# Performance work log

Hardware: AMD Instinct MI355X
Metric: run time of the kernel (lower is better)

Reference implementation:

```python
import jax, jax.numpy as jnp
import numpy as np

T, B, S, D = 128, 32, 100, 256  # targetL, batch, sourceL, output_size
EPS = 1e-6

def setup_inputs() -> dict:
    key = jax.random.key(0)
    ks = jax.random.split(key, 9)
    sc = 0.05  # weight init scale
    inp = {
        'prev_layer': jax.random.normal(ks[0], (T, B, D), dtype=jnp.float32),
        'hidden': jax.random.normal(ks[1], (B, D), dtype=jnp.float32),
        'enc_output': jax.random.normal(ks[2], (T * B, S, D), dtype=jnp.float32),
        # linear weights (layer_norm=True -> no biases on linears)
        'W_in': jax.random.normal(ks[3], (D, 3 * D), dtype=jnp.float32) * sc,
        'W_hid': jax.random.normal(ks[4], (D, D), dtype=jnp.float32) * sc,
        'W_ctx': jax.random.normal(ks[5], (D, D), dtype=jnp.float32) * sc,
        'W_enc': jax.random.normal(ks[6], (D, D), dtype=jnp.float32) * sc,
        'W_q': jax.random.normal(ks[7], (D, D), dtype=jnp.float32) * sc,   # MLPAttention query proj
        'v_att': jax.random.normal(ks[8], (D,), dtype=jnp.float32) * sc,  # MLPAttention score vector
        # layernorm affine params
        'g_pre': jnp.ones(3 * D, jnp.float32), 'b_pre': jnp.zeros(3 * D, jnp.float32),
        'g_enc': jnp.ones(D, jnp.float32), 'b_enc': jnp.zeros(D, jnp.float32),
        'g_h': jnp.ones(D, jnp.float32), 'b_h': jnp.zeros(D, jnp.float32),
        'g_c': jnp.ones(D, jnp.float32), 'b_c': jnp.zeros(D, jnp.float32),
        'g_q': jnp.ones(D, jnp.float32), 'b_q': jnp.zeros(D, jnp.float32),
    }
    return inp

def _ln(x, g, b):
    m = jnp.mean(x, axis=-1, keepdims=True)
    v = jnp.mean((x - m) ** 2, axis=-1, keepdims=True)
    return g * (x - m) / jnp.sqrt(v + EPS) + b

def reference(prev_layer, hidden, enc_output, W_in, W_hid, W_ctx, W_enc, W_q, v_att,
              g_pre, b_pre, g_enc, b_enc, g_h, b_h, g_c, b_c, g_q, b_q):
    Tl, Bb, Dd = prev_layer.shape
    # input / encoder projections (dropout=0 -> identity)
    preact = _ln(prev_layer @ W_in, g_pre, b_pre)        # [T,B,3D]
    pctx = _ln(enc_output @ W_enc, g_enc, b_enc)         # [T*B,S,D]
    z, h_gate, x_t = jnp.split(preact, 3, axis=-1)
    z = jax.nn.sigmoid(z)
    h_gate = jax.nn.sigmoid(h_gate)
    # SRU-style elementwise linear recurrence over time
    def step(h, zx):
        zt, xt = zx
        s = (1.0 - zt) * h + zt * xt
        return s, s
    final_h, ss = jax.lax.scan(step, hidden, (z, x_t))   # ss: [T,B,D]
    # MLP (Bahdanau) attention: scores = v . tanh(LN(Wq s) + pctx)
    q = _ln(ss @ W_q, g_q, b_q).reshape(Tl * Bb, 1, Dd)
    scores = jnp.einsum('nsd,d->ns', jnp.tanh(q + pctx), v_att)  # [T*B,S]
    attn = jax.nn.softmax(scores, axis=-1)
    attn_out = jnp.einsum('ns,nsd->nd', attn, pctx).reshape(Tl, Bb, Dd)
    attn_out = attn_out / np.sqrt(Dd).astype(np.float32)
    out = jnp.tanh(_ln(ss @ W_hid, g_h, b_h) + _ln(attn_out @ W_ctx, g_c, b_c))
    out = (1.0 - h_gate) * out + h_gate * prev_layer     # highway gate
    return out, final_h, attn
```

## Files before the change

### kernel.cpp

```cpp
#include <hip/hip_runtime.h>
#include <hip/hip_bf16.h>
#include <math.h>

typedef short  s16x8 __attribute__((ext_vector_type(8)));
typedef float  f32x4 __attribute__((ext_vector_type(4)));
typedef float  f32x2 __attribute__((ext_vector_type(2)));

#define LN_EPS 1e-6f

__device__ __forceinline__ unsigned short f2bf(float x) {
  union { float f; unsigned u; } v; v.f = x;
  unsigned r = v.u + 0x7FFFu + ((v.u >> 16) & 1u);
  return (unsigned short)(r >> 16);
}
__device__ __forceinline__ float bf2f(unsigned short u) {
  union { unsigned u; float f; } v; v.u = ((unsigned)u) << 16;
  return v.f;
}
__device__ __forceinline__ float bflo(unsigned u) {
  union { unsigned u; float f; } v; v.u = u << 16; return v.f;
}
__device__ __forceinline__ float bfhi(unsigned u) {
  union { unsigned u; float f; } v; v.u = u & 0xFFFF0000u; return v.f;
}
__device__ __forceinline__ unsigned pack_bf2(float a, float b) {
  __hip_bfloat162 h = __float22bfloat162_rn(make_float2(a, b));
  unsigned u; __builtin_memcpy(&u, &h, 4); return u;
}
__device__ __forceinline__ float fast_tanh(float x) {
  float e = __expf(2.0f * x);
  return 1.0f - 2.0f * __builtin_amdgcn_rcpf(e + 1.0f);
}
__device__ __forceinline__ float fast_sigmoid(float x) {
  return __builtin_amdgcn_rcpf(1.0f + __expf(-x));
}

template <int CTRL>
__device__ __forceinline__ float dpp_add(float v) {
  union { float f; int i; } a, r;
  a.f = v;
  r.i = __builtin_amdgcn_update_dpp(0, a.i, CTRL, 0xF, 0xF, true);
  return v + r.f;
}
template <int CTRL>
__device__ __forceinline__ float dpp_max(float v) {
  union { float f; int i; } a, r;
  a.f = v;
  r.i = __builtin_amdgcn_update_dpp(a.i, a.i, CTRL, 0xF, 0xF, false);
  return fmaxf(v, r.f);
}
__device__ __forceinline__ float bcast63(float v) {
  union { float f; int i; } a, r;
  a.f = v;
  r.i = __builtin_amdgcn_readlane(a.i, 63);
  return r.f;
}
__device__ __forceinline__ float wredsum(float v) {
  v = dpp_add<0x128>(v);
  v = dpp_add<0x124>(v);
  v = dpp_add<0x122>(v);
  v = dpp_add<0x121>(v);
  v = dpp_add<0x142>(v);
  v = dpp_add<0x143>(v);
  return bcast63(v);
}
__device__ __forceinline__ float wredmax(float v) {
  v = dpp_max<0x128>(v);
  v = dpp_max<0x124>(v);
  v = dpp_max<0x122>(v);
  v = dpp_max<0x121>(v);
  v = dpp_max<0x142>(v);
  v = dpp_max<0x143>(v);
  return bcast63(v);
}

__device__ __forceinline__ f32x4 mfma16(s16x8 a, s16x8 b, f32x4 c) {
  return __builtin_amdgcn_mfma_f32_16x16x32_bf16(a, b, c, 0, 0, 0);
}

__device__ __forceinline__ void stage_rows(unsigned short* A, const float* src,
                                           int rows, int tid, int nthreads) {
  char* Ab = (char*)A;
  int nquads = rows * 64;
  #pragma unroll 4
  for (int p = tid; p < nquads; p += nthreads) {
    int row = p >> 6, kq = p & 63;
    f32x4 v = *(const f32x4*)(src + row * 256 + kq * 4);
    unsigned u0 = pack_bf2(v.x, v.y);
    unsigned u1 = pack_bf2(v.z, v.w);
    int byte = row * 512 + ((kq * 8) ^ ((row & 7) << 4));
    *(uint2*)(Ab + byte) = uint2{u0, u1};
  }
}

__device__ __forceinline__ s16x8 readA(const unsigned short* A, int row, int kk, int hi) {
  const char* Ab = (const char*)A;
  int byte = row * 512 + (((kk * 64) + hi * 16) ^ ((row & 7) << 4));
  return *(const s16x8*)(Ab + byte);
}
__device__ __forceinline__ s16x8 readB(const unsigned short* Bt, int col, int kk, int hi) {
  return *(const s16x8*)(Bt + col * 256 + kk * 32 + hi * 8);
}

__global__ __launch_bounds__(256) void k_convw(
    const float* Win, const float* Wq, const float* Whid, const float* Wctx, const float* Wenc,
    unsigned short* bt_in, unsigned short* bt_q, unsigned short* bt_hid,
    unsigned short* bt_ctx, unsigned short* bt_enc) {
  __shared__ unsigned short tile[32][34];
  int b = blockIdx.x;
  const float* src; unsigned short* dst; int N, tk, tn;
  if (b < 192) { src = Win; dst = bt_in; N = 768; tk = b & 7; tn = b >> 3; }
  else {
    int bb = b - 192; int m = bb >> 6; int r = bb & 63;
    tk = r & 7; tn = r >> 3; N = 256;
    src = (m == 0) ? Wq : (m == 1) ? Whid : (m == 2) ? Wctx : Wenc;
    dst = (m == 0) ? bt_q : (m == 1) ? bt_hid : (m == 2) ? bt_ctx : bt_enc;
  }
  int k0 = tk * 32, n0 = tn * 32;
  {
    int i = threadIdx.x >> 3, j4 = (threadIdx.x & 7) * 4;
    f32x4 v = *(const f32x4*)(src + (size_t)(k0 + i) * N + n0 + j4);
    *(unsigned*)((char*)&tile[i][j4])     = pack_bf2(v.x, v.y);
    *(unsigned*)((char*)&tile[i][j4 + 2]) = pack_bf2(v.z, v.w);
  }
  __syncthreads();
  {
    int j = threadIdx.x >> 3, i4 = (threadIdx.x & 7) * 4;
    unsigned lo = (unsigned)tile[i4 + 0][j] | ((unsigned)tile[i4 + 1][j] << 16);
    unsigned hi = (unsigned)tile[i4 + 2][j] | ((unsigned)tile[i4 + 3][j] << 16);
    *(uint2*)(dst + (size_t)(n0 + j) * 256 + k0 + i4) = uint2{lo, hi};
  }
}

__global__ __launch_bounds__(256) void k_preact(
    const float* prev, const unsigned short* bt_in,
    const float* g_pre, const float* b_pre,
    float* Z, float* HG, float* XT) {
  __shared__ __align__(16) unsigned short A[16 * 256];
  __shared__ float C[16 * 768];
  int tid = threadIdx.x, lane = tid & 63, wave = tid >> 6;
  int hi = lane >> 4, lo = lane & 15;
  int r0 = blockIdx.x * 16;
  stage_rows(A, prev + (size_t)r0 * 256, 16, tid, 256);
  __syncthreads();
  f32x4 acc[12];
  #pragma unroll
  for (int ct = 0; ct < 12; ct++) acc[ct] = f32x4{0.f, 0.f, 0.f, 0.f};
  #pragma unroll
  for (int kk = 0; kk < 8; kk++) {
    s16x8 a = readA(A, lo, kk, hi);
    #pragma unroll
    for (int ct = 0; ct < 12; ct++) {
      s16x8 b = readB(bt_in, wave * 192 + ct * 16 + lo, kk, hi);
      acc[ct] = mfma16(a, b, acc[ct]);
    }
  }
  #pragma unroll
  for (int ct = 0; ct < 12; ct++) {
    int col = wave * 192 + ct * 16 + lo;
    #pragma unroll
    for (int r = 0; r < 4; r++) C[(hi * 4 + r) * 768 + col] = acc[ct][r];
  }
  __syncthreads();
  #pragma unroll
  for (int mm = 0; mm < 4; mm++) {
    int m = wave * 4 + mm;
    float x[12]; float s = 0.f, q = 0.f;
    #pragma unroll
    for (int i = 0; i < 12; i++) {
      x[i] = C[m * 768 + lane + 64 * i];
      s += x[i]; q += x[i] * x[i];
    }
    s = wredsum(s); q = wredsum(q);
    float mean = s * (1.0f / 768.0f);
    float var = q * (1.0f / 768.0f) - mean * mean;
    float rstd = rsqrtf(var + LN_EPS);
    int gr = r0 + m;
    #pragma unroll
    for (int i = 0; i < 12; i++) {
      int c = lane + 64 * i;
      float y = g_pre[c] * (x[i] - mean) * rstd + b_pre[c];
      if (c < 256)      Z [gr * 256 + c]         = fast_sigmoid(y);
      else if (c < 512) HG[gr * 256 + (c - 256)] = fast_sigmoid(y);
      else              XT[gr * 256 + (c - 512)] = y;
    }
  }
}

__global__ __launch_bounds__(256) void k_scan(
    const float* hidden, const float* Z, const float* XT,
    float* SS, float* outFinalH) {
  int tid = blockIdx.x * 256 + threadIdx.x;
  float h = hidden[tid];
  for (int t0 = 0; t0 < 128; t0 += 8) {
    float zc[8], xc[8];
    #pragma unroll
    for (int j = 0; j < 8; j++) {
      zc[j] = Z [(t0 + j) * 8192 + tid];
      xc[j] = XT[(t0 + j) * 8192 + tid];
    }
    #pragma unroll
    for (int j = 0; j < 8; j++) {
      h = (1.0f - zc[j]) * h + zc[j] * xc[j];
      SS[(t0 + j) * 8192 + tid] = h;
    }
  }
  outFinalH[tid] = h;
}

__global__ __launch_bounds__(256) void k_qproj(
    const float* SS, const unsigned short* bt_q,
    const float* g_q, const float* b_q, float* Q) {
  __shared__ __align__(16) unsigned short A[16 * 256];
  __shared__ float C[16 * 256];
  int tid = threadIdx.x, lane = tid & 63, wave = tid >> 6;
  int hi = lane >> 4, lo = lane & 15;
  int r0 = blockIdx.x * 16;
  stage_rows(A, SS + (size_t)r0 * 256, 16, tid, 256);
  __syncthreads();
  f32x4 acc[4];
  #pragma unroll
  for (int ct = 0; ct < 4; ct++) acc[ct] = f32x4{0.f, 0.f, 0.f, 0.f};
  #pragma unroll
  for (int kk = 0; kk < 8; kk++) {
    s16x8 a = readA(A, lo, kk, hi);
    #pragma unroll
    for (int ct = 0; ct < 4; ct++) {
      s16x8 b = readB(bt_q, wave * 64 + ct * 16 + lo, kk, hi);
      acc[ct] = mfma16(a, b, acc[ct]);
    }
  }
  #pragma unroll
  for (int ct = 0; ct < 4; ct++) {
    int col = wave * 64 + ct * 16 + lo;
    #pragma unroll
    for (int r = 0; r < 4; r++) C[(hi * 4 + r) * 256 + col] = acc[ct][r];
  }
  __syncthreads();
  #pragma unroll
  for (int mm = 0; mm < 4; mm++) {
    int m = wave * 4 + mm;
    float x[4]; float s = 0.f, q = 0.f;
    #pragma unroll
    for (int i = 0; i < 4; i++) {
      x[i] = C[m * 256 + lane + 64 * i];
      s += x[i]; q += x[i] * x[i];
    }
    s = wredsum(s); q = wredsum(q);
    float mean = s * (1.0f / 256.0f);
    float var = q * (1.0f / 256.0f) - mean * mean;
    float rstd = rsqrtf(var + LN_EPS);
    int gr = r0 + m;
    #pragma unroll
    for (int i = 0; i < 4; i++) {
      int c = lane + 64 * i;
      Q[gr * 256 + c] = g_q[c] * (x[i] - mean) * rstd + b_q[c];
    }
  }
}

__global__ __launch_bounds__(512, 6) void k_attn(
    const float* enc, const unsigned short* bt_enc, const float* Q,
    const float* g_enc, const float* b_enc, const float* v_att,
    float* AOUT, float* attnOut) {
  __shared__ __align__(16) unsigned short AP[100 * 256];
  __shared__ __align__(16) float alpha[112];
  __shared__ __align__(16) float stat[256];
  __shared__ float beta_s;
  int n = blockIdx.x;
  int tid = threadIdx.x, lane = tid & 63, wave = tid >> 6;
  int hi = lane >> 4, lo = lane & 15;
  stage_rows(AP, enc + (size_t)n * 25600, 100, tid, 512);
  __syncthreads();
  f32x4 acc[7][2];
  #pragma unroll
  for (int mt = 0; mt < 7; mt++) {
    acc[mt][0] = f32x4{0.f, 0.f, 0.f, 0.f};
    acc[mt][1] = f32x4{0.f, 0.f, 0.f, 0.f};
  }
  #pragma unroll
  for (int kk = 0; kk < 8; kk++) {
    s16x8 b0 = readB(bt_enc, wave * 32 + lo, kk, hi);
    s16x8 b1 = readB(bt_enc, wave * 32 + 16 + lo, kk, hi);
    #pragma unroll
    for (int mt = 0; mt < 7; mt++) {
      int ar = mt * 16 + lo;
      ar = ar > 99 ? 99 : ar;
      s16x8 a = readA(AP, ar, kk, hi);
      acc[mt][0] = mfma16(a, b0, acc[mt][0]);
      acc[mt][1] = mfma16(a, b1, acc[mt][1]);
    }
  }
  __syncthreads();
  #pragma unroll
  for (int mt = 0; mt < 7; mt++) {
    int col = wave * 32 + lo;
    #pragma unroll
    for (int r = 0; r < 4; r++) {
      int row = mt * 16 + hi * 4 + r;
      if (row < 100) {
        unsigned u = pack_bf2(acc[mt][0][r], acc[mt][1][r]);
        AP[row * 256 + col]      = (unsigned short)u;
        AP[row * 256 + col + 16] = (unsigned short)(u >> 16);
      }
    }
  }
  __syncthreads();
  {
    int ca = lane * 2;
    f32x2 gA = *(const f32x2*)(g_enc + ca), gB = *(const f32x2*)(g_enc + ca + 128);
    f32x2 bA = *(const f32x2*)(b_enc + ca), bB = *(const f32x2*)(b_enc + ca + 128);
    f32x2 vA = *(const f32x2*)(v_att + ca), vB = *(const f32x2*)(v_att + ca + 128);
    f32x2 qA = *(const f32x2*)(Q + (size_t)n * 256 + ca);
    f32x2 qB = *(const f32x2*)(Q + (size_t)n * 256 + ca + 128);
    #pragma unroll 2
    for (int m = wave; m < 100; m += 8) {
      const unsigned* Prow = (const unsigned*)(AP + m * 256);
      unsigned u01 = Prow[lane], u23 = Prow[lane + 64];
      float x0 = bflo(u01), x1 = bfhi(u01), x2 = bflo(u23), x3 = bfhi(u23);
      float s = (x0 + x1) + (x2 + x3);
      float q = fmaf(x0, x0, fmaf(x1, x1, fmaf(x2, x2, x3 * x3)));
      s = wredsum(s); q = wredsum(q);
      float mean = s * (1.0f / 256.0f);
      float var = q * (1.0f / 256.0f) - mean * mean;
      float rstd = rsqrtf(var + LN_EPS);
      float sc;
      sc  = vA.x * fast_tanh(qA.x + fmaf(gA.x, (x0 - mean) * rstd, bA.x));
      sc += vA.y * fast_tanh(qA.y + fmaf(gA.y, (x1 - mean) * rstd, bA.y));
      sc += vB.x * fast_tanh(qB.x + fmaf(gB.x, (x2 - mean) * rstd, bB.x));
      sc += vB.y * fast_tanh(qB.y + fmaf(gB.y, (x3 - mean) * rstd, bB.y));
      sc = wredsum(sc);
      if (lane == 0) { alpha[m] = sc; stat[m] = mean; stat[112 + m] = rstd; }
    }
  }
  __syncthreads();
  if (wave == 0) {
    float s1 = (lane < 100) ? alpha[lane] : -INFINITY;
    float s2 = (lane < 36)  ? alpha[lane + 64] : -INFINITY;
    float mx = wredmax(fmaxf(s1, s2));
    float e1 = (lane < 100) ? __expf(s1 - mx) : 0.f;
    float e2 = (lane < 36)  ? __expf(s2 - mx) : 0.f;
    float sm = wredsum(e1 + e2);
    float inv = __builtin_amdgcn_rcpf(sm);
    float p1 = e1 * inv, p2 = e2 * inv;
    float r1 = (lane < 100) ? stat[112 + lane] : 0.f;
    float m1 = (lane < 100) ? stat[lane] : 0.f;
    float r2 = (lane < 36)  ? stat[112 + lane + 64] : 0.f;
    float m2 = (lane < 36)  ? stat[lane + 64] : 0.f;
    float a1 = p1 * r1, a2 = p2 * r2;
    alpha[lane] = a1;
    if (lane < 48) alpha[lane + 64] = a2;
    float bp = wredsum(fmaf(a1, m1, a2 * m2));
    if (lane == 0) beta_s = bp;
    if (lane < 100) attnOut[(size_t)n * 100 + lane] = p1;
    if (lane < 36)  attnOut[(size_t)n * 100 + lane + 64] = p2;
  }
  __syncthreads();
  {
    int c = tid & 255, h = tid >> 8;
    float a = 0.f;
    #pragma unroll 5
    for (int s = h * 50; s < h * 50 + 50; s += 2) {
      f32x2 al = *(const f32x2*)(alpha + s);
      a = fmaf(al.x, bf2f(AP[s * 256 + c]), a);
      a = fmaf(al.y, bf2f(AP[(s + 1) * 256 + c]), a);
    }
    if (h == 1) stat[c] = a;
    __syncthreads();
    if (h == 0) {
      float S1 = a + stat[c];
      float y = fmaf(g_enc[c], S1 - beta_s, b_enc[c]);
      AOUT[(size_t)n * 256 + c] = y * 0.0625f;
    }
  }
}

__global__ __launch_bounds__(256) void k_out(
    const float* SS, const float* AOUT,
    const unsigned short* bt_hid, const unsigned short* bt_ctx,
    const float* g_h, const float* b_h, const float* g_c, const float* b_c,
    const float* HG, const float* prev, float* out) {
  __shared__ __align__(16) unsigned short A1[16 * 256];
  __shared__ __align__(16) unsigned short A2[16 * 256];
  __shared__ float C1[16 * 256];
  __shared__ float C2[16 * 256];
  int tid = threadIdx.x, lane = tid & 63, wave = tid >> 6;
  int hi = lane >> 4, lo = lane & 15;
  int r0 = blockIdx.x * 16;
  stage_rows(A1, SS + (size_t)r0 * 256, 16, tid, 256);
  stage_rows(A2, AOUT + (size_t)r0 * 256, 16, tid, 256);
  __syncthreads();
  f32x4 acc1[4], acc2[4];
  #pragma unroll
  for (int ct = 0; ct < 4; ct++) {
    acc1[ct] = f32x4{0.f, 0.f, 0.f, 0.f};
    acc2[ct] = f32x4{0.f, 0.f, 0.f, 0.f};
  }
  #pragma unroll
  for (int kk = 0; kk < 8; kk++) {
    s16x8 a1 = readA(A1, lo, kk, hi);
    s16x8 a2 = readA(A2, lo, kk, hi);
    #pragma unroll
    for (int ct = 0; ct < 4; ct++) {
      int col = wave * 64 + ct * 16 + lo;
      s16x8 b1 = readB(bt_hid, col, kk, hi);
      s16x8 b2 = readB(bt_ctx, col, kk, hi);
      acc1[ct] = mfma16(a1, b1, acc1[ct]);
      acc2[ct] = mfma16(a2, b2, acc2[ct]);
    }
  }
  #pragma unroll
  for (int ct = 0; ct < 4; ct++) {
    int col = wave * 64 + ct * 16 + lo;
    #pragma unroll
    for (int r = 0; r < 4; r++) {
      C1[(hi * 4 + r) * 256 + col] = acc1[ct][r];
      C2[(hi * 4 + r) * 256 + col] = acc2[ct][r];
    }
  }
  __syncthreads();
  #pragma unroll
  for (int mm = 0; mm < 4; mm++) {
    int m = wave * 4 + mm;
    float x1[4], x2[4];
    float s1 = 0.f, q1 = 0.f, s2 = 0.f, q2 = 0.f;
    #pragma unroll
    for (int i = 0; i < 4; i++) {
      x1[i] = C1[m * 256 + lane + 64 * i];
      x2[i] = C2[m * 256 + lane + 64 * i];
      s1 += x1[i]; q1 += x1[i] * x1[i];
      s2 += x2[i]; q2 += x2[i] * x2[i];
    }
    s1 = wredsum(s1); q1 = wredsum(q1);
    s2 = wredsum(s2); q2 = wredsum(q2);
    float mean1 = s1 * (1.0f / 256.0f), var1 = q1 * (1.0f / 256.0f) - mean1 * mean1;
    float mean2 = s2 * (1.0f / 256.0f), var2 = q2 * (1.0f / 256.0f) - mean2 * mean2;
    float rstd1 = rsqrtf(var1 + LN_EPS), rstd2 = rsqrtf(var2 + LN_EPS);
    int gr = r0 + m;
    #pragma unroll
    for (int i = 0; i < 4; i++) {
      int c = lane + 64 * i;
      float y1 = g_h[c] * (x1[i] - mean1) * rstd1 + b_h[c];
      float y2 = g_c[c] * (x2[i] - mean2) * rstd2 + b_c[c];
      float y = fast_tanh(y1 + y2);
      float g = HG[gr * 256 + c];
      float pv = prev[gr * 256 + c];
      out[gr * 256 + c] = (1.0f - g) * y + g * pv;
    }
  }
}

extern "C" void kernel_launch(void* const* d_in, const int* in_sizes, int n_in,
                              void* d_out, int out_size, void* d_ws, size_t ws_size,
                              hipStream_t stream) {
  const float* prev   = (const float*)d_in[0];
  const float* hidden = (const float*)d_in[1];
  const float* enc    = (const float*)d_in[2];
  const float* W_in   = (const float*)d_in[3];
  const float* W_hid  = (const float*)d_in[4];
  const float* W_ctx  = (const float*)d_in[5];
  const float* W_enc  = (const float*)d_in[6];
  const float* W_q    = (const float*)d_in[7];
  const float* v_att  = (const float*)d_in[8];
  const float* g_pre  = (const float*)d_in[9];
  const float* b_pre  = (const float*)d_in[10];
  const float* g_enc  = (const float*)d_in[11];
  const float* b_enc  = (const float*)d_in[12];
  const float* g_h    = (const float*)d_in[13];
  const float* b_h    = (const float*)d_in[14];
  const float* g_c    = (const float*)d_in[15];
  const float* b_c    = (const float*)d_in[16];
  const float* g_q    = (const float*)d_in[17];
  const float* b_q    = (const float*)d_in[18];

  char* ws = (char*)d_ws;
  unsigned short* BT_IN  = (unsigned short*)(ws + 0);
  unsigned short* BT_Q   = (unsigned short*)(ws + 393216);
  unsigned short* BT_HID = (unsigned short*)(ws + 524288);
  unsigned short* BT_CTX = (unsigned short*)(ws + 655360);
  unsigned short* BT_ENC = (unsigned short*)(ws + 786432);
  float* Z    = (float*)(ws + 917504);
  float* HG   = (float*)(ws + 5111808);
  float* XT   = (float*)(ws + 9306112);
  float* SS   = (float*)(ws + 13500416);
  float* Q    = (float*)(ws + 17694720);
  float* AOUT = (float*)(ws + 21889024);

  float* out    = (float*)d_out;
  float* finalH = out + 1048576;
  float* attnO  = out + 1056768;

  k_convw <<<448, 256, 0, stream>>>(W_in, W_q, W_hid, W_ctx, W_enc,
                                    BT_IN, BT_Q, BT_HID, BT_CTX, BT_ENC);
  k_preact<<<256, 256, 0, stream>>>(prev, BT_IN, g_pre, b_pre, Z, HG, XT);
  k_scan  <<<32, 256, 0, stream>>>(hidden, Z, XT, SS, finalH);
  k_qproj <<<256, 256, 0, stream>>>(SS, BT_Q, g_q, b_q, Q);
  k_attn  <<<4096, 512, 0, stream>>>(enc, BT_ENC, Q, g_enc, b_enc, v_att, AOUT, attnO);
  k_out   <<<256, 256, 0, stream>>>(SS, AOUT, BT_HID, BT_CTX,
                                    g_h, b_h, g_c, b_c, HG, prev, out);
}
```

Baseline: 289.5 us.

## Keep attention projection in MFMA registers and reduce LayerNorm/score stats across waves

The k_attn epilogue no longer writes the projected encoder tile back to LDS as bf16 and re-reads it per row. Instead, each wave packs its MFMA accumulators into registers and computes per-row partial sums and sums of squares with 16-lane DPP reductions. Those partials are combined across the 8 waves through small LDS buffers that reuse the AP region, and the score and weighted-sum phases are then driven from the same registers. W_enc columns are permuted during weight conversion so each lane owns two adjacent output columns, which allows vectorised parameter loads and f32x2 output stores. The change also unrolls the enc staging loop. In exchange it adds extra barriers and cross-wave partial buffers and raises register pressure from keeping 28 packed values live.

```diff
diff --git a/kernel.cpp b/kernel.cpp
--- a/kernel.cpp
+++ b/kernel.cpp
@@ -56,22 +56,18 @@
   return r.f;
 }
 __device__ __forceinline__ float wredsum(float v) {
-  v = dpp_add<0x128>(v);
-  v = dpp_add<0x124>(v);
-  v = dpp_add<0x122>(v);
-  v = dpp_add<0x121>(v);
-  v = dpp_add<0x142>(v);
-  v = dpp_add<0x143>(v);
+  v = dpp_add<0x128>(v); v = dpp_add<0x124>(v); v = dpp_add<0x122>(v); v = dpp_add<0x121>(v);
+  v = dpp_add<0x142>(v); v = dpp_add<0x143>(v);
   return bcast63(v);
 }
 __device__ __forceinline__ float wredmax(float v) {
-  v = dpp_max<0x128>(v);
-  v = dpp_max<0x124>(v);
-  v = dpp_max<0x122>(v);
-  v = dpp_max<0x121>(v);
-  v = dpp_max<0x142>(v);
-  v = dpp_max<0x143>(v);
+  v = dpp_max<0x128>(v); v = dpp_max<0x124>(v); v = dpp_max<0x122>(v); v = dpp_max<0x121>(v);
+  v = dpp_max<0x142>(v); v = dpp_max<0x143>(v);
   return bcast63(v);
+}
+__device__ __forceinline__ float red16(float v) {
+  v = dpp_add<0x121>(v); v = dpp_add<0x122>(v); v = dpp_add<0x124>(v); v = dpp_add<0x128>(v);
+  return v;
 }
 
 __device__ __forceinline__ f32x4 mfma16(s16x8 a, s16x8 b, f32x4 c) {
@@ -108,13 +104,14 @@
     unsigned short* bt_ctx, unsigned short* bt_enc) {
   __shared__ unsigned short tile[32][34];
   int b = blockIdx.x;
-  const float* src; unsigned short* dst; int N, tk, tn;
+  const float* src; unsigned short* dst; int N, tk, tn; bool perm = false;
   if (b < 192) { src = Win; dst = bt_in; N = 768; tk = b & 7; tn = b >> 3; }
   else {
     int bb = b - 192; int m = bb >> 6; int r = bb & 63;
     tk = r & 7; tn = r >> 3; N = 256;
     src = (m == 0) ? Wq : (m == 1) ? Whid : (m == 2) ? Wctx : Wenc;
     dst = (m == 0) ? bt_q : (m == 1) ? bt_hid : (m == 2) ? bt_ctx : bt_enc;
+    perm = (m == 3);
   }
   int k0 = tk * 32, n0 = tn * 32;
   {
@@ -126,9 +123,11 @@
   __syncthreads();
   {
     int j = threadIdx.x >> 3, i4 = (threadIdx.x & 7) * 4;
+    int c = n0 + j;
+    int dr = perm ? ((c & ~31) | ((c & 31) >> 1) | ((c & 1) << 4)) : c;
     unsigned lo = (unsigned)tile[i4 + 0][j] | ((unsigned)tile[i4 + 1][j] << 16);
     unsigned hi = (unsigned)tile[i4 + 2][j] | ((unsigned)tile[i4 + 3][j] << 16);
-    *(uint2*)(dst + (size_t)(n0 + j) * 256 + k0 + i4) = uint2{lo, hi};
+    *(uint2*)(dst + (size_t)dr * 256 + k0 + i4) = uint2{lo, hi};
   }
 }
 
@@ -265,12 +264,34 @@
     float* AOUT, float* attnOut) {
   __shared__ __align__(16) unsigned short AP[100 * 256];
   __shared__ __align__(16) float alpha[112];
-  __shared__ __align__(16) float stat[256];
+  __shared__ __align__(16) f32x2 stats[112];
   __shared__ float beta_s;
+  f32x2* statp = (f32x2*)AP;
+  float* spart = (float*)((char*)AP + 16384);
   int n = blockIdx.x;
   int tid = threadIdx.x, lane = tid & 63, wave = tid >> 6;
   int hi = lane >> 4, lo = lane & 15;
-  stage_rows(AP, enc + (size_t)n * 25600, 100, tid, 512);
+  {
+    const float* src = enc + (size_t)n * 25600;
+    char* Ab = (char*)AP;
+    #pragma unroll
+    for (int i = 0; i < 12; i++) {
+      int p = tid + i * 512;
+      int row = p >> 6, kq = p & 63;
+      f32x4 v = *(const f32x4*)(src + row * 256 + kq * 4);
+      unsigned u0 = pack_bf2(v.x, v.y), u1 = pack_bf2(v.z, v.w);
+      int byte = row * 512 + ((kq * 8) ^ ((row & 7) << 4));
+      *(uint2*)(Ab + byte) = uint2{u0, u1};
+    }
+    if (tid < 256) {
+      int p = 6144 + tid;
+      int row = p >> 6, kq = p & 63;
+      f32x4 v = *(const f32x4*)(src + row * 256 + kq * 4);
+      unsigned u0 = pack_bf2(v.x, v.y), u1 = pack_bf2(v.z, v.w);
+      int byte = row * 512 + ((kq * 8) ^ ((row & 7) << 4));
+      *(uint2*)(Ab + byte) = uint2{u0, u1};
+    }
+  }
   __syncthreads();
   f32x4 acc[7][2];
   #pragma unroll
@@ -292,86 +313,97 @@
     }
   }
   __syncthreads();
+  unsigned pk[7][4];
   #pragma unroll
   for (int mt = 0; mt < 7; mt++) {
-    int col = wave * 32 + lo;
+    #pragma unroll
+    for (int r = 0; r < 4; r++) {
+      unsigned u = pack_bf2(acc[mt][0][r], acc[mt][1][r]);
+      pk[mt][r] = u;
+      float x0 = bflo(u), x1 = bfhi(u);
+      float s = red16(x0 + x1);
+      float q = red16(fmaf(x0, x0, x1 * x1));
+      if (lo == 0) statp[wave * 112 + mt * 16 + hi * 4 + r] = f32x2{s, q};
+    }
+  }
+  __syncthreads();
+  if (tid < 112) {
+    float S = 0.f, Qs = 0.f;
+    #pragma unroll
+    for (int w = 0; w < 8; w++) {
+      f32x2 t = statp[w * 112 + tid];
+      S += t.x; Qs += t.y;
+    }
+    float mean = S * (1.0f / 256.0f);
+    float var = Qs * (1.0f / 256.0f) - mean * mean;
+    stats[tid] = f32x2{mean, rsqrtf(var + LN_EPS)};
+  }
+  __syncthreads();
+  int c0 = (wave << 5) + (lo << 1);
+  f32x2 gp = *(const f32x2*)(g_enc + c0);
+  f32x2 bp = *(const f32x2*)(b_enc + c0);
+  f32x2 vp = *(const f32x2*)(v_att + c0);
+  f32x2 qp = *(const f32x2*)(Q + (size_t)n * 256 + c0);
+  #pragma unroll
+  for (int mt = 0; mt < 7; mt++) {
     #pragma unroll
     for (int r = 0; r < 4; r++) {
       int row = mt * 16 + hi * 4 + r;
-      if (row < 100) {
-        unsigned u = pack_bf2(acc[mt][0][r], acc[mt][1][r]);
-        AP[row * 256 + col]      = (unsigned short)u;
-        AP[row * 256 + col + 16] = (unsigned short)(u >> 16);
-      }
-    }
-  }
-  __syncthreads();
-  {
-    int ca = lane * 2;
-    f32x2 gA = *(const f32x2*)(g_enc + ca), gB = *(const f32x2*)(g_enc + ca + 128);
-    f32x2 bA = *(const f32x2*)(b_enc + ca), bB = *(const f32x2*)(b_enc + ca + 128);
-    f32x2 vA = *(const f32x2*)(v_att + ca), vB = *(const f32x2*)(v_att + ca + 128);
-    f32x2 qA = *(const f32x2*)(Q + (size_t)n * 256 + ca);
-    f32x2 qB = *(const f32x2*)(Q + (size_t)n * 256 + ca + 128);
-    #pragma unroll 2
-    for (int m = wave; m < 100; m += 8) {
-      const unsigned* Prow = (const unsigned*)(AP + m * 256);
-      unsigned u01 = Prow[lane], u23 = Prow[lane + 64];
-      float x0 = bflo(u01), x1 = bfhi(u01), x2 = bflo(u23), x3 = bfhi(u23);
-      float s = (x0 + x1) + (x2 + x3);
-      float q = fmaf(x0, x0, fmaf(x1, x1, fmaf(x2, x2, x3 * x3)));
-      s = wredsum(s); q = wredsum(q);
-      float mean = s * (1.0f / 256.0f);
-      float var = q * (1.0f / 256.0f) - mean * mean;
-      float rstd = rsqrtf(var + LN_EPS);
-      float sc;
-      sc  = vA.x * fast_tanh(qA.x + fmaf(gA.x, (x0 - mean) * rstd, bA.x));
-      sc += vA.y * fast_tanh(qA.y + fmaf(gA.y, (x1 - mean) * rstd, bA.y));
-      sc += vB.x * fast_tanh(qB.x + fmaf(gB.x, (x2 - mean) * rstd, bB.x));
-      sc += vB.y * fast_tanh(qB.y + fmaf(gB.y, (x3 - mean) * rstd, bB.y));
-      sc = wredsum(sc);
-      if (lane == 0) { alpha[m] = sc; stat[m] = mean; stat[112 + m] = rstd; }
+      f32x2 st = stats[row];
+      float x0 = bflo(pk[mt][r]), x1 = bfhi(pk[mt][r]);
+      float t = vp.x * fast_tanh(qp.x + fmaf(gp.x, (x0 - st.x) * st.y, bp.x))
+              + vp.y * fast_tanh(qp.y + fmaf(gp.y, (x1 - st.x) * st.y, bp.y));
+      t = red16(t);
+      if (lo == 0) spart[wave * 112 + row] = t;
     }
   }
   __syncthreads();
   if (wave == 0) {
-    float s1 = (lane < 100) ? alpha[lane] : -INFINITY;
-    float s2 = (lane < 36)  ? alpha[lane + 64] : -INFINITY;
+    int row2 = (lane < 36) ? lane + 64 : lane;
+    float s1 = 0.f, s2 = 0.f;
+    #pragma unroll
+    for (int w = 0; w < 8; w++) {
+      s1 += spart[w * 112 + lane];
+      s2 += spart[w * 112 + row2];
+    }
+    s2 = (lane < 36) ? s2 : -INFINITY;
     float mx = wredmax(fmaxf(s1, s2));
-    float e1 = (lane < 100) ? __expf(s1 - mx) : 0.f;
-    float e2 = (lane < 36)  ? __expf(s2 - mx) : 0.f;
+    float e1 = __expf(s1 - mx);
+    float e2 = (lane < 36) ? __expf(s2 - mx) : 0.f;
     float sm = wredsum(e1 + e2);
     float inv = __builtin_amdgcn_rcpf(sm);
     float p1 = e1 * inv, p2 = e2 * inv;
-    float r1 = (lane < 100) ? stat[112 + lane] : 0.f;
-    float m1 = (lane < 100) ? stat[lane] : 0.f;
-    float r2 = (lane < 36)  ? stat[112 + lane + 64] : 0.f;
-    float m2 = (lane < 36)  ? stat[lane + 64] : 0.f;
-    float a1 = p1 * r1, a2 = p2 * r2;
+    f32x2 st1 = stats[lane];
+    float a1 = p1 * st1.y, bsum = a1 * st1.x;
+    float a2 = 0.f;
+    if (lane < 36) {
+      f32x2 st2 = stats[lane + 64];
+      a2 = p2 * st2.y; bsum = fmaf(a2, st2.x, bsum);
+    }
     alpha[lane] = a1;
     if (lane < 48) alpha[lane + 64] = a2;
-    float bp = wredsum(fmaf(a1, m1, a2 * m2));
-    if (lane == 0) beta_s = bp;
-    if (lane < 100) attnOut[(size_t)n * 100 + lane] = p1;
-    if (lane < 36)  attnOut[(size_t)n * 100 + lane + 64] = p2;
-  }
-  __syncthreads();
-  {
-    int c = tid & 255, h = tid >> 8;
-    float a = 0.f;
-    #pragma unroll 5
-    for (int s = h * 50; s < h * 50 + 50; s += 2) {
-      f32x2 al = *(const f32x2*)(alpha + s);
-      a = fmaf(al.x, bf2f(AP[s * 256 + c]), a);
-      a = fmaf(al.y, bf2f(AP[(s + 1) * 256 + c]), a);
-    }
-    if (h == 1) stat[c] = a;
-    __syncthreads();
-    if (h == 0) {
-      float S1 = a + stat[c];
-      float y = fmaf(g_enc[c], S1 - beta_s, b_enc[c]);
-      AOUT[(size_t)n * 256 + c] = y * 0.0625f;
-    }
+    float bp_ = wredsum(bsum);
+    if (lane == 0) beta_s = bp_;
+    attnOut[(size_t)n * 100 + lane] = p1;
+    if (lane < 36) attnOut[(size_t)n * 100 + lane + 64] = p2;
+  }
+  __syncthreads();
+  float w0 = 0.f, w1 = 0.f;
+  #pragma unroll
+  for (int mt = 0; mt < 7; mt++) {
+    f32x4 al = *(const f32x4*)(alpha + mt * 16 + hi * 4);
+    #pragma unroll
+    for (int r = 0; r < 4; r++) {
+      w0 = fmaf(al[r], bflo(pk[mt][r]), w0);
+      w1 = fmaf(al[r], bfhi(pk[mt][r]), w1);
+    }
+  }
+  w0 += __shfl_xor(w0, 16); w0 += __shfl_xor(w0, 32);
+  w1 += __shfl_xor(w1, 16); w1 += __shfl_xor(w1, 32);
+  if (lane < 16) {
+    float y0 = fmaf(gp.x, w0 - beta_s, bp.x) * 0.0625f;
+    float y1 = fmaf(gp.y, w1 - beta_s, bp.y) * 0.0625f;
+    *(f32x2*)(AOUT + (size_t)n * 256 + c0) = f32x2{y0, y1};
   }
 }
 
```

Result: slower. 458.0 us (+58.2%).
